# Optimization experiments

Measured on AMD Instinct MI355X. Metric: run time of the kernel, lower is better.

Reference implementation:

```python
import jax, jax.numpy as jnp
import numpy as np

N_HEAD = 16

def setup_inputs() -> dict:
    key = jax.random.key(0)
    ks = jax.random.split(key, 5)
    C = 1024
    s = 1.0 / np.sqrt(C)
    x = jax.random.normal(ks[0], (2, 2048, C), dtype=jnp.float32)
    wq = jax.random.normal(ks[1], (C, C), dtype=jnp.float32) * s
    wk = jax.random.normal(ks[2], (C, C), dtype=jnp.float32) * s
    wv = jax.random.normal(ks[3], (C, C), dtype=jnp.float32) * s
    wp = jax.random.normal(ks[4], (C, C), dtype=jnp.float32) * s
    z = jnp.zeros((C,), dtype=jnp.float32)
    return {"x": x, "wq": wq, "bq": z, "wk": wk, "bk": z,
            "wv": wv, "bv": z, "wp": wp, "bp": z}

def reference(x, wq, bq, wk, bk, wv, bv, wp, bp):
    B, T, C = x.shape
    H = N_HEAD
    D = C // H
    # projections: weights stored as (in, out) -> x @ w + b
    q = (x @ wq + bq).reshape(B, T, H, D).transpose(0, 2, 1, 3)  # [B,H,T,D]
    k = (x @ wk + bk).reshape(B, T, H, D).transpose(0, 2, 1, 3)
    v = (x @ wv + bv).reshape(B, T, H, D).transpose(0, 2, 1, 3)
    att = jnp.einsum('bhqd,bhkd->bhqk', q, k) / jnp.sqrt(jnp.float32(D))
    causal = jnp.tril(jnp.ones((T, T), dtype=bool))
    att = jnp.where(causal[None, None], att, -jnp.inf)
    att = jax.nn.softmax(att, axis=-1)
    out = jnp.einsum('bhqk,bhkd->bhqd', att, v)  # [B,H,T,D]
    out = out.transpose(0, 2, 1, 3).reshape(B, T, C)
    return out @ wp + bp
```

## Files before the change

### kernel.cpp

```cpp
#include <hip/hip_runtime.h>
#include <hip/hip_bf16.h>
#include <stdint.h>


typedef __attribute__((ext_vector_type(8))) short bf16x8;
typedef __attribute__((ext_vector_type(4))) float f32x4;
typedef __attribute__((ext_vector_type(4))) short short4v;

#define MFMA16(a,b,c) __builtin_amdgcn_mfma_f32_16x16x32_bf16(a,b,c,0,0,0)

__device__ __forceinline__ unsigned short f2bfu(float f){
  union { __hip_bfloat16 h; unsigned short u; } cv;
  cv.h = __float2bfloat16(f);
  return cv.u;
}

__device__ __forceinline__ unsigned cvtpk(float a, float b){
  unsigned r;
  asm("v_cvt_pk_bf16_f32 %0, %1, %2" : "=v"(r) : "v"(a), "v"(b));
  return r;
}

__device__ __forceinline__ void async16(const void* g, void* s){
  __builtin_amdgcn_global_load_lds((const __attribute__((address_space(1))) void*)g,
                                   (__attribute__((address_space(3))) void*)s, 16, 0, 0);
}

__global__ __launch_bounds__(256)
void prep_k(const float* __restrict__ x, unsigned short* __restrict__ xb,
            const float* __restrict__ wq, const float* __restrict__ wk,
            const float* __restrict__ wv, const float* __restrict__ wp,
            unsigned short* __restrict__ wqkvT, unsigned short* __restrict__ wpT)
{
  __shared__ float t[32][33];
  const int bx = blockIdx.x;
  const int tid = threadIdx.x;
  if (bx < 4096) {
    const int i = bx * 256 + tid;
    const float4 v = ((const float4*)x)[i];
    short4v o;
    o.x = (short)f2bfu(v.x); o.y = (short)f2bfu(v.y);
    o.z = (short)f2bfu(v.z); o.w = (short)f2bfu(v.w);
    ((short4v*)xb)[i] = o;
    return;
  }
  const int b = bx - 4096;
  const int wsel = b >> 10;
  const float* W = (wsel == 0) ? wq : (wsel == 1) ? wk : (wsel == 2) ? wv : wp;
  unsigned short* Wt = (wsel == 3) ? wpT : wqkvT + (size_t)wsel * 1024 * 1024;
  const int bc = ((b & 1023) & 31) * 32;
  const int br = ((b & 1023) >> 5) * 32;
  const int tx = tid & 31, ty = tid >> 5;
  #pragma unroll
  for (int i = 0; i < 32; i += 8)
    t[ty + i][tx] = W[(size_t)(br + ty + i) * 1024 + bc + tx];
  __syncthreads();
  #pragma unroll
  for (int i = 0; i < 32; i += 8)
    Wt[(size_t)(bc + ty + i) * 1024 + br + tx] = f2bfu(t[tx][ty + i]);
}

template<int MODE>
__global__ __launch_bounds__(256)
void gemm_bt(const unsigned short* __restrict__ A, const unsigned short* __restrict__ Bt,
             const float* __restrict__ b0, const float* __restrict__ b1, const float* __restrict__ b2,
             unsigned short* __restrict__ Qo, unsigned short* __restrict__ Ko,
             unsigned short* __restrict__ Vo, float* __restrict__ Fo, int N)
{
  constexpr int K = 1024;
  __shared__ unsigned short As[2][128 * 32];
  __shared__ unsigned short Bs[2][128 * 32];
  const int tid = threadIdx.x;
  const int lane = tid & 63;
  const int w = tid >> 6;
  const int l15 = lane & 15, lhi = lane >> 4;
  const int row0 = blockIdx.y * 128;
  const int col0 = blockIdx.x * 128;
  const int wr = (w >> 1) * 64;
  const int wc = (w & 1) * 64;

  f32x4 acc[4][4];
  #pragma unroll
  for (int i = 0; i < 4; i++)
    #pragma unroll
    for (int j = 0; j < 4; j++) acc[i][j] = 0.0f;

  const int srow = lane >> 2;
  const int scol = (lane & 3) * 8;
  const unsigned short* Ab = A  + (size_t)(row0 + w * 32 + srow) * K + scol;
  const unsigned short* Bb = Bt + (size_t)(col0 + w * 32 + srow) * K + scol;
  const int wofs = (w * 32) * 32;

  auto stageg = [&](int k0, int buf) {
    async16(Ab + k0,          &As[buf][wofs]);
    async16(Ab + k0 + 16 * K, &As[buf][wofs + 16 * 32]);
    async16(Bb + k0,          &Bs[buf][wofs]);
    async16(Bb + k0 + 16 * K, &Bs[buf][wofs + 16 * 32]);
  };

  stageg(0, 0);
  __syncthreads();
  int cur = 0;
  for (int k0 = 0; k0 < K; k0 += 32) {
    if (k0 + 32 < K) stageg(k0 + 32, cur ^ 1);
    bf16x8 af[4], bfv[4];
    #pragma unroll
    for (int i = 0; i < 4; i++) {
      af[i]  = *(const bf16x8*)&As[cur][(wr + i * 16 + l15) * 32 + lhi * 8];
      bfv[i] = *(const bf16x8*)&Bs[cur][(wc + i * 16 + l15) * 32 + lhi * 8];
    }
    __builtin_amdgcn_s_setprio(1);
    #pragma unroll
    for (int i = 0; i < 4; i++)
      #pragma unroll
      for (int j = 0; j < 4; j++)
        acc[i][j] = MFMA16(af[i], bfv[j], acc[i][j]);
    __builtin_amdgcn_s_setprio(0);
    __syncthreads();
    cur ^= 1;
  }

  #pragma unroll
  for (int j = 0; j < 4; j++) {
    const int n = col0 + wc + j * 16 + l15;
    if constexpr (MODE == 0) {
      const int which = n >> 10;
      const int cn = n & 1023;
      const float bias = (which == 0 ? b0[cn] : which == 1 ? b1[cn] : b2[cn]);
      const int h = cn >> 6, d = cn & 63;
      if (which == 2) {
        #pragma unroll
        for (int i = 0; i < 4; i++) {
          const int m = row0 + wr + i * 16 + lhi * 4;
          const int b_ = m >> 11, t = m & 2047;
          uint2 pk;
          pk.x = cvtpk(acc[i][j][0] + bias, acc[i][j][1] + bias);
          pk.y = cvtpk(acc[i][j][2] + bias, acc[i][j][3] + bias);
          *(uint2*)(Vo + (((size_t)(b_ * 16 + h) * 64 + d) * 2048 + t)) = pk;
        }
      } else {
        unsigned short* dst = (which == 0 ? Qo : Ko);
        const float sc = (which == 0 ? 0.125f * 1.44269504f : 1.0f);
        #pragma unroll
        for (int i = 0; i < 4; i++)
          #pragma unroll
          for (int r = 0; r < 4; r++) {
            const int m = row0 + wr + i * 16 + lhi * 4 + r;
            const int b_ = m >> 11, t = m & 2047;
            dst[(((size_t)(b_ * 16 + h) * 2048 + t) * 64) + d] =
                f2bfu((acc[i][j][r] + bias) * sc);
          }
      }
    } else {
      const float bias = b0[n];
      #pragma unroll
      for (int i = 0; i < 4; i++)
        #pragma unroll
        for (int r = 0; r < 4; r++) {
          const int m = row0 + wr + i * 16 + lhi * 4 + r;
          Fo[(size_t)m * N + n] = acc[i][j][r] + bias;
        }
    }
  }
}


__device__ __forceinline__ void softmax_pack(
    f32x4 (&s)[4], f32x4 (&o)[4], float& mrun, float& lrun,
    unsigned short* __restrict__ Pw, int l15, int lhi, int q0, int kv0, bool mask)
{
  if (mask) {
    const int q = q0 + l15;
    #pragma unroll
    for (int nf = 0; nf < 4; ++nf)
      #pragma unroll
      for (int r = 0; r < 4; r++) {
        const int kv = kv0 + nf * 16 + lhi * 4 + r;
        if (kv > q) s[nf][r] = -1e30f;
      }
  }
  float m0 = fmaxf(fmaxf(s[0][0], s[0][1]), fmaxf(s[0][2], s[0][3]));
  float m1 = fmaxf(fmaxf(s[1][0], s[1][1]), fmaxf(s[1][2], s[1][3]));
  float m2 = fmaxf(fmaxf(s[2][0], s[2][1]), fmaxf(s[2][2], s[2][3]));
  float m3 = fmaxf(fmaxf(s[3][0], s[3][1]), fmaxf(s[3][2], s[3][3]));
  float pm = fmaxf(fmaxf(m0, m1), fmaxf(m2, m3));
  pm = fmaxf(pm, __shfl_xor(pm, 16, 64));
  pm = fmaxf(pm, __shfl_xor(pm, 32, 64));

  if (__any((int)(pm > mrun + 8.0f))) {
    const float mnew = fmaxf(mrun, pm);
    const float sc = exp2f(mrun - mnew);
    mrun = mnew;
    lrun *= sc;
    float scr[4];
    #pragma unroll
    for (int r = 0; r < 4; r++) scr[r] = __shfl(sc, lhi * 4 + r, 64);
    #pragma unroll
    for (int nf = 0; nf < 4; nf++)
      #pragma unroll
      for (int r = 0; r < 4; r++) o[nf][r] *= scr[r];
  }

  float rs = 0.0f;
  const int swz = (l15 & 7) << 4;
  #pragma unroll
  for (int nf = 0; nf < 4; nf++) {
    float p0 = exp2f(s[nf][0] - mrun);
    float p1 = exp2f(s[nf][1] - mrun);
    float p2 = exp2f(s[nf][2] - mrun);
    float p3 = exp2f(s[nf][3] - mrun);
    rs += (p0 + p1) + (p2 + p3);
    uint2 pk;
    pk.x = cvtpk(p0, p1);
    pk.y = cvtpk(p2, p3);
    *(uint2*)((char*)Pw + ((l15 * 128 + nf * 32 + lhi * 8) ^ swz)) = pk;
  }
  rs += __shfl_xor(rs, 16, 64);
  rs += __shfl_xor(rs, 32, 64);
  lrun += rs;
}

__global__ __launch_bounds__(256)
void attn_k(const unsigned short* __restrict__ Q, const unsigned short* __restrict__ Kg,
            const unsigned short* __restrict__ VT, unsigned short* __restrict__ O)
{
  __shared__ unsigned short Ks[2][64 * 64];
  __shared__ unsigned short Vs[2][64 * 64];
  __shared__ alignas(16) unsigned short Ps[4][2048];
  const int flat = blockIdx.y * 16 + blockIdx.x;
  const int u = (flat & 7) * 64 + (flat >> 3);
  const int bx = u & 15, bh = u >> 4;
  const int b_ = bh >> 4, h = bh & 15;
  const int tid = threadIdx.x, lane = tid & 63, w = tid >> 6;
  const int l15 = lane & 15, lhi = lane >> 4;
  const int tA = bx * 4 + w, tB = 127 - tA;
  const int q0A = tA * 16, q0B = tB * 16;
  const int jmA = bx, jmB = 31 - bx;

  const unsigned short* Kbh  = Kg + (size_t)bh * (2048 * 64);
  const unsigned short* VTbh = VT + (size_t)bh * (64 * 2048);
  unsigned short* PwB = &Ps[w][0];
  unsigned short* PwA = &Ps[w][1024];

  const unsigned short* QpA = Q + ((size_t)bh * 2048 + q0A + l15) * 64 + lhi * 8;
  const unsigned short* QpB = Q + ((size_t)bh * 2048 + q0B + l15) * 64 + lhi * 8;
  const bf16x8 qfA0 = *(const bf16x8*)(QpA);
  const bf16x8 qfA1 = *(const bf16x8*)(QpA + 32);
  const bf16x8 qfB0 = *(const bf16x8*)(QpB);
  const bf16x8 qfB1 = *(const bf16x8*)(QpB + 32);

  f32x4 oA[4], oB[4];
  #pragma unroll
  for (int nf = 0; nf < 4; nf++) { oA[nf] = 0.0f; oB[nf] = 0.0f; }
  float mA = -1e30f, lA = 0.0f, mB = -1e30f, lB = 0.0f;

  const int srow = w * 8 + (lane >> 3);
  const int cole = (((lane & 7) ^ (lane >> 3)) << 3);
  const unsigned short* Ksrc = Kbh + (size_t)srow * 64 + cole;
  const unsigned short* Vsrc = VTbh + (size_t)srow * 2048 + cole;

  auto stage = [&](int kv0, int buf) {
    unsigned short* kb = &Ks[buf][w * 512];
    unsigned short* vb = &Vs[buf][w * 512];
    #pragma unroll
    for (int it = 0; it < 2; ++it) {
      async16(Ksrc + (size_t)(kv0 + it * 32) * 64, kb + it * 2048);
      async16(Vsrc + (size_t)(it * 32) * 2048 + kv0, vb + it * 2048);
    }
  };

  stage(0, 0);
  __syncthreads();

  int cur = 0;
  for (int j = 0; j <= jmB; ++j) {
    if (j < jmB) stage((j + 1) * 64, cur ^ 1);
    const int kv0 = j * 64;
    const bool doA = (j <= jmA);
    const unsigned short* Ksb = &Ks[cur][0];
    const unsigned short* Vsb = &Vs[cur][0];

    f32x4 sB[4], sA[4];
    __builtin_amdgcn_s_setprio(1);
    #pragma unroll
    for (int nf = 0; nf < 4; ++nf) {
      const int rk = nf * 16 + l15;
      const int swzk = (rk & 7) << 4;
      const bf16x8 kf0 = *(const bf16x8*)((const char*)Ksb + ((rk * 128 + lhi * 16) ^ swzk));
      const bf16x8 kf1 = *(const bf16x8*)((const char*)Ksb + ((rk * 128 + 64 + lhi * 16) ^ swzk));
      sB[nf] = 0.0f;
      sB[nf] = MFMA16(kf0, qfB0, sB[nf]);
      sB[nf] = MFMA16(kf1, qfB1, sB[nf]);
      if (doA) {
        sA[nf] = 0.0f;
        sA[nf] = MFMA16(kf0, qfA0, sA[nf]);
        sA[nf] = MFMA16(kf1, qfA1, sA[nf]);
      }
    }
    __builtin_amdgcn_s_setprio(0);

    softmax_pack(sB, oB, mB, lB, PwB, l15, lhi, q0B, kv0, j == jmB);
    if (doA) softmax_pack(sA, oA, mA, lA, PwA, l15, lhi, q0A, kv0, j == jmA);

    const int swzp = (l15 & 7) << 4;
    const bf16x8 pfB0 = *(const bf16x8*)((const char*)PwB + ((l15 * 128 + lhi * 16) ^ swzp));
    const bf16x8 pfB1 = *(const bf16x8*)((const char*)PwB + ((l15 * 128 + 64 + lhi * 16) ^ swzp));
    bf16x8 pfA0, pfA1;
    if (doA) {
      pfA0 = *(const bf16x8*)((const char*)PwA + ((l15 * 128 + lhi * 16) ^ swzp));
      pfA1 = *(const bf16x8*)((const char*)PwA + ((l15 * 128 + 64 + lhi * 16) ^ swzp));
    }

    __builtin_amdgcn_s_setprio(1);
    #pragma unroll
    for (int nf = 0; nf < 4; nf++) {
      const int rv = nf * 16 + l15;
      const int swzv = (rv & 7) << 4;
      const bf16x8 vf0 = *(const bf16x8*)((const char*)Vsb + ((rv * 128 + lhi * 16) ^ swzv));
      const bf16x8 vf1 = *(const bf16x8*)((const char*)Vsb + ((rv * 128 + 64 + lhi * 16) ^ swzv));
      oB[nf] = MFMA16(pfB0, vf0, oB[nf]);
      oB[nf] = MFMA16(pfB1, vf1, oB[nf]);
      if (doA) {
        oA[nf] = MFMA16(pfA0, vf0, oA[nf]);
        oA[nf] = MFMA16(pfA1, vf1, oA[nf]);
      }
    }
    __builtin_amdgcn_s_setprio(0);

    __syncthreads();
    cur ^= 1;
  }

  const float linvA = 1.0f / lA, linvB = 1.0f / lB;
  float invA[4], invB[4];
  #pragma unroll
  for (int r = 0; r < 4; r++) {
    invA[r] = __shfl(linvA, lhi * 4 + r, 64);
    invB[r] = __shfl(linvB, lhi * 4 + r, 64);
  }
  #pragma unroll
  for (int nf = 0; nf < 4; nf++)
    #pragma unroll
    for (int r = 0; r < 4; r++) {
      const int c = h * 64 + nf * 16 + l15;
      O[((size_t)b_ * 2048 + q0A + lhi * 4 + r) * 1024 + c] = f2bfu(oA[nf][r] * invA[r]);
      O[((size_t)b_ * 2048 + q0B + lhi * 4 + r) * 1024 + c] = f2bfu(oB[nf][r] * invB[r]);
    }
}


extern "C" void kernel_launch(void* const* d_in, const int* in_sizes, int n_in,
                              void* d_out, int out_size, void* d_ws, size_t ws_size,
                              hipStream_t stream) {
  const float* x  = (const float*)d_in[0];
  const float* wq = (const float*)d_in[1];
  const float* bq = (const float*)d_in[2];
  const float* wk = (const float*)d_in[3];
  const float* bk = (const float*)d_in[4];
  const float* wv = (const float*)d_in[5];
  const float* bv = (const float*)d_in[6];
  const float* wp = (const float*)d_in[7];
  const float* bp = (const float*)d_in[8];
  float* out = (float*)d_out;

  char* ws = (char*)d_ws;
  const size_t MB = 1024 * 1024;
  unsigned short* xb    = (unsigned short*)(ws);
  unsigned short* wqkvT = (unsigned short*)(ws + 8  * MB);
  unsigned short* wpT   = (unsigned short*)(ws + 14 * MB);
  unsigned short* Qb    = (unsigned short*)(ws + 16 * MB);
  unsigned short* Kb    = (unsigned short*)(ws + 24 * MB);
  unsigned short* VTb   = (unsigned short*)(ws + 32 * MB);
  unsigned short* Ob    = (unsigned short*)(ws);

  prep_k<<<dim3(8192), dim3(256), 0, stream>>>(x, xb, wq, wk, wv, wp, wqkvT, wpT);

  gemm_bt<0><<<dim3(24, 32), dim3(256), 0, stream>>>(xb, wqkvT, bq, bk, bv,
                                                     Qb, Kb, VTb, nullptr, 3072);
  attn_k<<<dim3(16, 32), dim3(256), 0, stream>>>(Qb, Kb, VTb, Ob);
  gemm_bt<1><<<dim3(8, 32), dim3(256), 0, stream>>>(Ob, wpT, bp, nullptr, nullptr,
                                                    nullptr, nullptr, nullptr, out, 1024);
}
```

Measured before the change: 127.2 us.

## Switch attention to 32x32 MFMA tiles with register-resident P via permlane swap

Rewrites the attention kernel to use 32x32x16 bf16 MFMA with 32-row query tiles per wave, halving the grid to 256 blocks. The softmax probabilities are packed to bf16 and rearranged in registers with v_permlane32_swap instead of going through a shared-memory round trip. The output is written with packed 8-byte stores. Fewer blocks and launch_bounds(256,1) raise register use and may lower occupancy or leave CUs idle.

```diff
diff --git a/kernel.cpp b/kernel.cpp
--- a/kernel.cpp
+++ b/kernel.cpp
@@ -3,11 +3,13 @@
 #include <stdint.h>
 
 
-typedef __attribute__((ext_vector_type(8))) short bf16x8;
-typedef __attribute__((ext_vector_type(4))) float f32x4;
-typedef __attribute__((ext_vector_type(4))) short short4v;
+typedef __attribute__((ext_vector_type(8)))  short bf16x8;
+typedef __attribute__((ext_vector_type(4)))  float f32x4;
+typedef __attribute__((ext_vector_type(16))) float f32x16;
+typedef __attribute__((ext_vector_type(4)))  short short4v;
 
 #define MFMA16(a,b,c) __builtin_amdgcn_mfma_f32_16x16x32_bf16(a,b,c,0,0,0)
+#define MFMA32(a,b,c) __builtin_amdgcn_mfma_f32_32x32x16_bf16(a,b,c,0,0,0)
 
 __device__ __forceinline__ unsigned short f2bfu(float f){
   union { __hip_bfloat16 h; unsigned short u; } cv;
@@ -19,6 +21,10 @@
   unsigned r;
   asm("v_cvt_pk_bf16_f32 %0, %1, %2" : "=v"(r) : "v"(a), "v"(b));
   return r;
+}
+
+__device__ __forceinline__ void permswap(unsigned &x, unsigned &y){
+  asm volatile("v_permlane32_swap_b32 %0, %1" : "+v"(x), "+v"(y));
 }
 
 __device__ __forceinline__ void async16(const void* g, void* s){
@@ -165,94 +171,47 @@
 }
 
 
-__device__ __forceinline__ void softmax_pack(
-    f32x4 (&s)[4], f32x4 (&o)[4], float& mrun, float& lrun,
-    unsigned short* __restrict__ Pw, int l15, int lhi, int q0, int kv0, bool mask)
-{
-  if (mask) {
-    const int q = q0 + l15;
-    #pragma unroll
-    for (int nf = 0; nf < 4; ++nf)
-      #pragma unroll
-      for (int r = 0; r < 4; r++) {
-        const int kv = kv0 + nf * 16 + lhi * 4 + r;
-        if (kv > q) s[nf][r] = -1e30f;
-      }
-  }
-  float m0 = fmaxf(fmaxf(s[0][0], s[0][1]), fmaxf(s[0][2], s[0][3]));
-  float m1 = fmaxf(fmaxf(s[1][0], s[1][1]), fmaxf(s[1][2], s[1][3]));
-  float m2 = fmaxf(fmaxf(s[2][0], s[2][1]), fmaxf(s[2][2], s[2][3]));
-  float m3 = fmaxf(fmaxf(s[3][0], s[3][1]), fmaxf(s[3][2], s[3][3]));
-  float pm = fmaxf(fmaxf(m0, m1), fmaxf(m2, m3));
-  pm = fmaxf(pm, __shfl_xor(pm, 16, 64));
-  pm = fmaxf(pm, __shfl_xor(pm, 32, 64));
-
-  if (__any((int)(pm > mrun + 8.0f))) {
-    const float mnew = fmaxf(mrun, pm);
-    const float sc = exp2f(mrun - mnew);
-    mrun = mnew;
-    lrun *= sc;
-    float scr[4];
-    #pragma unroll
-    for (int r = 0; r < 4; r++) scr[r] = __shfl(sc, lhi * 4 + r, 64);
-    #pragma unroll
-    for (int nf = 0; nf < 4; nf++)
-      #pragma unroll
-      for (int r = 0; r < 4; r++) o[nf][r] *= scr[r];
-  }
-
-  float rs = 0.0f;
-  const int swz = (l15 & 7) << 4;
-  #pragma unroll
-  for (int nf = 0; nf < 4; nf++) {
-    float p0 = exp2f(s[nf][0] - mrun);
-    float p1 = exp2f(s[nf][1] - mrun);
-    float p2 = exp2f(s[nf][2] - mrun);
-    float p3 = exp2f(s[nf][3] - mrun);
-    rs += (p0 + p1) + (p2 + p3);
-    uint2 pk;
-    pk.x = cvtpk(p0, p1);
-    pk.y = cvtpk(p2, p3);
-    *(uint2*)((char*)Pw + ((l15 * 128 + nf * 32 + lhi * 8) ^ swz)) = pk;
-  }
-  rs += __shfl_xor(rs, 16, 64);
-  rs += __shfl_xor(rs, 32, 64);
-  lrun += rs;
-}
-
-__global__ __launch_bounds__(256)
+__global__ __launch_bounds__(256, 1)
 void attn_k(const unsigned short* __restrict__ Q, const unsigned short* __restrict__ Kg,
             const unsigned short* __restrict__ VT, unsigned short* __restrict__ O)
 {
   __shared__ unsigned short Ks[2][64 * 64];
   __shared__ unsigned short Vs[2][64 * 64];
-  __shared__ alignas(16) unsigned short Ps[4][2048];
-  const int flat = blockIdx.y * 16 + blockIdx.x;
-  const int u = (flat & 7) * 64 + (flat >> 3);
-  const int bx = u & 15, bh = u >> 4;
+  const int flat = blockIdx.y * 8 + blockIdx.x;
+  const int u = (flat & 7) * 32 + (flat >> 3);
+  const int bx = u & 7, bh = u >> 3;
   const int b_ = bh >> 4, h = bh & 15;
   const int tid = threadIdx.x, lane = tid & 63, w = tid >> 6;
-  const int l15 = lane & 15, lhi = lane >> 4;
-  const int tA = bx * 4 + w, tB = 127 - tA;
-  const int q0A = tA * 16, q0B = tB * 16;
-  const int jmA = bx, jmB = 31 - bx;
+  const int r0 = lane & 31, hi5 = lane >> 5;
+  const int p  = bx * 4 + w;
+  const int pB = 63 - p;
+  const int q0A = p * 32, q0B = pB * 32;
+  const int jmA = p >> 1, jmB = pB >> 1;
+  const int jmax = (63 - bx * 4) >> 1;
 
   const unsigned short* Kbh  = Kg + (size_t)bh * (2048 * 64);
   const unsigned short* VTbh = VT + (size_t)bh * (64 * 2048);
-  unsigned short* PwB = &Ps[w][0];
-  unsigned short* PwA = &Ps[w][1024];
-
-  const unsigned short* QpA = Q + ((size_t)bh * 2048 + q0A + l15) * 64 + lhi * 8;
-  const unsigned short* QpB = Q + ((size_t)bh * 2048 + q0B + l15) * 64 + lhi * 8;
-  const bf16x8 qfA0 = *(const bf16x8*)(QpA);
-  const bf16x8 qfA1 = *(const bf16x8*)(QpA + 32);
-  const bf16x8 qfB0 = *(const bf16x8*)(QpB);
-  const bf16x8 qfB1 = *(const bf16x8*)(QpB + 32);
-
-  f32x4 oA[4], oB[4];
-  #pragma unroll
-  for (int nf = 0; nf < 4; nf++) { oA[nf] = 0.0f; oB[nf] = 0.0f; }
+
+  bf16x8 qfA[4], qfB[4];
+  {
+    const unsigned short* QA = Q + ((size_t)bh * 2048 + q0A + r0) * 64 + hi5 * 8;
+    const unsigned short* QB = Q + ((size_t)bh * 2048 + q0B + r0) * 64 + hi5 * 8;
+    #pragma unroll
+    for (int s = 0; s < 4; s++) {
+      qfA[s] = *(const bf16x8*)(QA + s * 16);
+      qfB[s] = *(const bf16x8*)(QB + s * 16);
+    }
+  }
+
+  f32x16 oA[2], oB[2];
+  #pragma unroll
+  for (int d = 0; d < 2; d++) { oA[d] = 0.0f; oB[d] = 0.0f; }
   float mA = -1e30f, lA = 0.0f, mB = -1e30f, lB = 0.0f;
+
+  int fragoff[4];
+  #pragma unroll
+  for (int t = 0; t < 4; t++)
+    fragoff[t] = (r0 * 128 + t * 32 + hi5 * 16) ^ ((r0 & 7) << 4);
 
   const int srow = w * 8 + (lane >> 3);
   const int cole = (((lane & 7) ^ (lane >> 3)) << 3);
@@ -269,83 +228,122 @@
     }
   };
 
+  const unsigned short* Ksb;
+  const unsigned short* Vsb;
+
+  auto member = [&](f32x16 (&oT)[2], const bf16x8 (&qf)[4],
+                    float& mrun, float& lrun, int q0, int kv0, bool mask) {
+    f32x16 s0 = 0.0f, s1 = 0.0f;
+    __builtin_amdgcn_s_setprio(1);
+    #pragma unroll
+    for (int t = 0; t < 4; t++) {
+      const bf16x8 ka = *(const bf16x8*)((const char*)Ksb + fragoff[t]);
+      const bf16x8 kb = *(const bf16x8*)((const char*)Ksb + fragoff[t] + 4096);
+      s0 = MFMA32(ka, qf[t], s0);
+      s1 = MFMA32(kb, qf[t], s1);
+    }
+    __builtin_amdgcn_s_setprio(0);
+
+    const int q = q0 + r0;
+    if (mask) {
+      #pragma unroll
+      for (int r = 0; r < 16; r++) {
+        const int kvr = kv0 + (r & 3) + 8 * (r >> 2) + 4 * hi5;
+        if (kvr      > q) s0[r] = -1e30f;
+        if (kvr + 32 > q) s1[r] = -1e30f;
+      }
+    }
+
+    float pm = fmaxf(s0[0], s1[0]);
+    #pragma unroll
+    for (int r = 1; r < 16; r++) pm = fmaxf(pm, fmaxf(s0[r], s1[r]));
+    pm = fmaxf(pm, __shfl_xor(pm, 32, 64));
+
+    if (__any((int)(pm > mrun + 8.0f))) {
+      const float mnew = fmaxf(mrun, pm);
+      const float sc = exp2f(mrun - mnew);
+      mrun = mnew; lrun *= sc;
+      oT[0] *= sc; oT[1] *= sc;
+    }
+
+    float p0[16], p1[16];
+    float rs = 0.0f;
+    #pragma unroll
+    for (int r = 0; r < 16; r++) {
+      p0[r] = exp2f(s0[r] - mrun);
+      p1[r] = exp2f(s1[r] - mrun);
+      rs += p0[r] + p1[r];
+    }
+    rs += __shfl_xor(rs, 32, 64);
+    lrun += rs;
+
+    bf16x8 pb[4];
+    #pragma unroll
+    for (int sub = 0; sub < 2; sub++) {
+      {
+        unsigned a = cvtpk(p0[sub*8+0], p0[sub*8+1]);
+        unsigned b = cvtpk(p0[sub*8+2], p0[sub*8+3]);
+        unsigned c = cvtpk(p0[sub*8+4], p0[sub*8+5]);
+        unsigned d = cvtpk(p0[sub*8+6], p0[sub*8+7]);
+        permswap(a, c); permswap(b, d);
+        union { unsigned u[4]; bf16x8 hv; } wv_;
+        wv_.u[0] = a; wv_.u[1] = b; wv_.u[2] = c; wv_.u[3] = d;
+        pb[sub] = wv_.hv;
+      }
+      {
+        unsigned a = cvtpk(p1[sub*8+0], p1[sub*8+1]);
+        unsigned b = cvtpk(p1[sub*8+2], p1[sub*8+3]);
+        unsigned c = cvtpk(p1[sub*8+4], p1[sub*8+5]);
+        unsigned d = cvtpk(p1[sub*8+6], p1[sub*8+7]);
+        permswap(a, c); permswap(b, d);
+        union { unsigned u[4]; bf16x8 hv; } wv_;
+        wv_.u[0] = a; wv_.u[1] = b; wv_.u[2] = c; wv_.u[3] = d;
+        pb[2 + sub] = wv_.hv;
+      }
+    }
+
+    __builtin_amdgcn_s_setprio(1);
+    #pragma unroll
+    for (int t = 0; t < 4; t++) {
+      const bf16x8 va = *(const bf16x8*)((const char*)Vsb + fragoff[t]);
+      const bf16x8 vb = *(const bf16x8*)((const char*)Vsb + fragoff[t] + 4096);
+      oT[0] = MFMA32(va, pb[t], oT[0]);
+      oT[1] = MFMA32(vb, pb[t], oT[1]);
+    }
+    __builtin_amdgcn_s_setprio(0);
+  };
+
   stage(0, 0);
   __syncthreads();
 
   int cur = 0;
-  for (int j = 0; j <= jmB; ++j) {
-    if (j < jmB) stage((j + 1) * 64, cur ^ 1);
+  for (int j = 0; j <= jmax; ++j) {
+    if (j < jmax) stage((j + 1) * 64, cur ^ 1);
+    Ksb = &Ks[cur][0];
+    Vsb = &Vs[cur][0];
     const int kv0 = j * 64;
-    const bool doA = (j <= jmA);
-    const unsigned short* Ksb = &Ks[cur][0];
-    const unsigned short* Vsb = &Vs[cur][0];
-
-    f32x4 sB[4], sA[4];
-    __builtin_amdgcn_s_setprio(1);
-    #pragma unroll
-    for (int nf = 0; nf < 4; ++nf) {
-      const int rk = nf * 16 + l15;
-      const int swzk = (rk & 7) << 4;
-      const bf16x8 kf0 = *(const bf16x8*)((const char*)Ksb + ((rk * 128 + lhi * 16) ^ swzk));
-      const bf16x8 kf1 = *(const bf16x8*)((const char*)Ksb + ((rk * 128 + 64 + lhi * 16) ^ swzk));
-      sB[nf] = 0.0f;
-      sB[nf] = MFMA16(kf0, qfB0, sB[nf]);
-      sB[nf] = MFMA16(kf1, qfB1, sB[nf]);
-      if (doA) {
-        sA[nf] = 0.0f;
-        sA[nf] = MFMA16(kf0, qfA0, sA[nf]);
-        sA[nf] = MFMA16(kf1, qfA1, sA[nf]);
-      }
-    }
-    __builtin_amdgcn_s_setprio(0);
-
-    softmax_pack(sB, oB, mB, lB, PwB, l15, lhi, q0B, kv0, j == jmB);
-    if (doA) softmax_pack(sA, oA, mA, lA, PwA, l15, lhi, q0A, kv0, j == jmA);
-
-    const int swzp = (l15 & 7) << 4;
-    const bf16x8 pfB0 = *(const bf16x8*)((const char*)PwB + ((l15 * 128 + lhi * 16) ^ swzp));
-    const bf16x8 pfB1 = *(const bf16x8*)((const char*)PwB + ((l15 * 128 + 64 + lhi * 16) ^ swzp));
-    bf16x8 pfA0, pfA1;
-    if (doA) {
-      pfA0 = *(const bf16x8*)((const char*)PwA + ((l15 * 128 + lhi * 16) ^ swzp));
-      pfA1 = *(const bf16x8*)((const char*)PwA + ((l15 * 128 + 64 + lhi * 16) ^ swzp));
-    }
-
-    __builtin_amdgcn_s_setprio(1);
-    #pragma unroll
-    for (int nf = 0; nf < 4; nf++) {
-      const int rv = nf * 16 + l15;
-      const int swzv = (rv & 7) << 4;
-      const bf16x8 vf0 = *(const bf16x8*)((const char*)Vsb + ((rv * 128 + lhi * 16) ^ swzv));
-      const bf16x8 vf1 = *(const bf16x8*)((const char*)Vsb + ((rv * 128 + 64 + lhi * 16) ^ swzv));
-      oB[nf] = MFMA16(pfB0, vf0, oB[nf]);
-      oB[nf] = MFMA16(pfB1, vf1, oB[nf]);
-      if (doA) {
-        oA[nf] = MFMA16(pfA0, vf0, oA[nf]);
-        oA[nf] = MFMA16(pfA1, vf1, oA[nf]);
-      }
-    }
-    __builtin_amdgcn_s_setprio(0);
-
+    if (j <= jmB) member(oB, qfB, mB, lB, q0B, kv0, j == jmB);
+    if (j <= jmA) member(oA, qfA, mA, lA, q0A, kv0, j == jmA);
     __syncthreads();
     cur ^= 1;
   }
 
-  const float linvA = 1.0f / lA, linvB = 1.0f / lB;
-  float invA[4], invB[4];
-  #pragma unroll
-  for (int r = 0; r < 4; r++) {
-    invA[r] = __shfl(linvA, lhi * 4 + r, 64);
-    invB[r] = __shfl(linvB, lhi * 4 + r, 64);
-  }
-  #pragma unroll
-  for (int nf = 0; nf < 4; nf++)
-    #pragma unroll
-    for (int r = 0; r < 4; r++) {
-      const int c = h * 64 + nf * 16 + l15;
-      O[((size_t)b_ * 2048 + q0A + lhi * 4 + r) * 1024 + c] = f2bfu(oA[nf][r] * invA[r]);
-      O[((size_t)b_ * 2048 + q0B + lhi * 4 + r) * 1024 + c] = f2bfu(oB[nf][r] * invB[r]);
-    }
+  auto emit = [&](f32x16 (&oT)[2], float lr, int q0) {
+    const float linv = 1.0f / lr;
+    const int q = q0 + r0;
+    unsigned short* obase = O + ((size_t)b_ * 2048 + q) * 1024 + h * 64 + hi5 * 4;
+    #pragma unroll
+    for (int dh = 0; dh < 2; dh++)
+      #pragma unroll
+      for (int g = 0; g < 4; g++) {
+        uint2 pk;
+        pk.x = cvtpk(oT[dh][4*g]   * linv, oT[dh][4*g+1] * linv);
+        pk.y = cvtpk(oT[dh][4*g+2] * linv, oT[dh][4*g+3] * linv);
+        *(uint2*)(obase + dh * 32 + g * 8) = pk;
+      }
+  };
+  emit(oA, lA, q0A);
+  emit(oB, lB, q0B);
 }
 
 
@@ -377,7 +375,7 @@
 
   gemm_bt<0><<<dim3(24, 32), dim3(256), 0, stream>>>(xb, wqkvT, bq, bk, bv,
                                                      Qb, Kb, VTb, nullptr, 3072);
-  attn_k<<<dim3(16, 32), dim3(256), 0, stream>>>(Qb, Kb, VTb, Ob);
+  attn_k<<<dim3(8, 32), dim3(256), 0, stream>>>(Qb, Kb, VTb, Ob);
   gemm_bt<1><<<dim3(8, 32), dim3(256), 0, stream>>>(Ob, wpT, bp, nullptr, nullptr,
                                                     nullptr, nullptr, nullptr, out, 1024);
 }
```

Result: slower. 143.4 us (+12.8%).
